# Performance work log

Measured on AMD Instinct MI355X. Metric: run time of the kernel, lower is better.

## Reference

```python
import jax, jax.numpy as jnp
import numpy as np
import itertools

GRID = 256          # voxel grid extent per axis (coords in [0, GRID))
KSIZE = 3           # kernel_size
OFFSETS = np.array(list(itertools.product(range(KSIZE), repeat=3)), dtype=np.int32) - (KSIZE // 2)  # [27,3]


def setup_inputs() -> dict:
    key = jax.random.key(0)
    k1, k2, k3 = jax.random.split(key, 3)
    N, Cin, Cout = 262144, 64, 64
    coords = jax.random.randint(k1, (N, 3), 0, GRID, dtype=jnp.int32)
    feats = jax.random.normal(k2, (N, Cin), dtype=jnp.float32)
    kernel = jax.random.normal(k3, (KSIZE ** 3, Cin, Cout), dtype=jnp.float32) * 0.02
    return {"coords": coords, "feats": feats, "kernel": kernel}


def reference(coords, feats, kernel):
    # Submanifold sparse conv3d: out[i] = sum_k feats[j_k(i)] @ kernel[k]
    # where coords[j_k(i)] == coords[i] + offset_k (if such a point exists).
    N = coords.shape[0]
    Cout = kernel.shape[-1]
    # Hash table: linearized voxel -> point index (-1 if empty).
    lin = (coords[:, 0] * GRID + coords[:, 1]) * GRID + coords[:, 2]
    table = jnp.full((GRID ** 3,), -1, dtype=jnp.int32).at[lin].set(
        jnp.arange(N, dtype=jnp.int32))
    out = jnp.zeros((N, Cout), dtype=feats.dtype)
    for k in range(KSIZE ** 3):
        off = jnp.asarray(OFFSETS[k])              # [3]
        nc = coords + off[None, :]                 # neighbor coords [N,3]
        in_bounds = jnp.all((nc >= 0) & (nc < GRID), axis=1)
        nlin = (nc[:, 0] * GRID + nc[:, 1]) * GRID + nc[:, 2]
        idx = table[jnp.clip(nlin, 0, GRID ** 3 - 1)]
        valid = in_bounds & (idx >= 0)
        g = feats[jnp.where(valid, idx, 0)] * valid[:, None].astype(feats.dtype)  # [N,Cin]
        out = out + g @ kernel[k]                  # [N,Cout]
    return out
```

## Files before the change

### kernel.cpp

```cpp
#include <hip/hip_runtime.h>

#define VGRID 256
#define N_TAPS 27
#define CIN 64
#define COUT 64
#define PAIR_CAP 32768
#define CNT_STRIDE 16
#define LCAP 64

typedef __attribute__((ext_vector_type(8))) short short8;
typedef __attribute__((ext_vector_type(4))) float float4v;

__device__ __forceinline__ short f2bf(float x) {
    unsigned u = __builtin_bit_cast(unsigned, x);
    unsigned r = (u + 0x7FFF + ((u >> 16) & 1)) >> 16;
    return (short)r;
}

__global__ void build_table_kernel(const int* __restrict__ coords,
                                   int* __restrict__ table, int n) {
    int i = blockIdx.x * blockDim.x + threadIdx.x;
    if (i >= n) return;
    int cx = coords[i * 3 + 0];
    int cy = coords[i * 3 + 1];
    int cz = coords[i * 3 + 2];
    int lin = (cx * VGRID + cy) * VGRID + cz;
    atomicMax(&table[lin], i);
}

__global__ void __launch_bounds__(256) probe_kernel(
        const int* __restrict__ coords, const int* __restrict__ table,
        int* __restrict__ counters, int2* __restrict__ pairs,
        int* __restrict__ jc, int n) {
    __shared__ int lcnt[26];
    __shared__ int lbase[26];
    __shared__ int2 lpairs[26][LCAP];

    int t = threadIdx.x;
    int i = blockIdx.x * 256 + t;
    if (t < 26) lcnt[t] = 0;
    __syncthreads();

    if (i < n) {
        int cx = coords[i * 3 + 0];
        int cy = coords[i * 3 + 1];
        int cz = coords[i * 3 + 2];
        int idxs[N_TAPS];
#pragma unroll
        for (int k = 0; k < N_TAPS; ++k) {
            int ox = k / 9 - 1, oy = (k / 3) % 3 - 1, oz = k % 3 - 1;
            int nx = cx + ox, ny = cy + oy, nz = cz + oz;
            bool v = ((unsigned)nx < VGRID) && ((unsigned)ny < VGRID) &&
                     ((unsigned)nz < VGRID);
            idxs[k] = v ? table[(nx * VGRID + ny) * VGRID + nz] : -1;
        }
        jc[i] = idxs[13];
#pragma unroll
        for (int k = 0; k < N_TAPS; ++k) {
            if (k == 13) continue;
            if (idxs[k] >= 0) {
                int kidx = k - (k > 13);
                int pos = atomicAdd(&lcnt[kidx], 1);
                if (pos < LCAP) lpairs[kidx][pos] = make_int2(i, idxs[k]);
            }
        }
    }
    __syncthreads();

    if (t < 26) {
        int c = lcnt[t];
        if (c > LCAP) c = LCAP;
        lcnt[t] = c;
        lbase[t] = atomicAdd(&counters[t * CNT_STRIDE], c);
    }
    __syncthreads();

    int wave = t >> 6, lane = t & 63;
    for (int k = wave; k < 26; k += 4) {
        int c = lcnt[k];
        if (lane < c) {
            int pos = lbase[k] + lane;
            if (pos < PAIR_CAP) pairs[(size_t)k * PAIR_CAP + pos] = lpairs[k][lane];
        }
    }
}

__global__ void __launch_bounds__(256) center_gemm_kernel(
        const float* __restrict__ feats, const float* __restrict__ weights,
        const int* __restrict__ jc, float* __restrict__ out, int n) {
    __shared__ short a_lds[64][CIN + 8];
    int base = blockIdx.x * 64;
    int t = threadIdx.x;

    {
        int r = t >> 2;
        int seg = (t & 3) * 16;
        int row = base + r;
        int j = (row < n) ? jc[row] : 0;
        const float4* src = (const float4*)(feats + (size_t)j * CIN + seg);
#pragma unroll
        for (int q = 0; q < 4; ++q) {
            float4 v = src[q];
            a_lds[r][seg + q * 4 + 0] = f2bf(v.x);
            a_lds[r][seg + q * 4 + 1] = f2bf(v.y);
            a_lds[r][seg + q * 4 + 2] = f2bf(v.z);
            a_lds[r][seg + q * 4 + 3] = f2bf(v.w);
        }
    }
    __syncthreads();

    int wave = t >> 6, lane = t & 63;
    int quad = lane >> 4, m = lane & 15;
    const float* W = weights + 13 * CIN * COUT;
    int row0 = wave * 16;

#pragma unroll
    for (int nt = 0; nt < 4; ++nt) {
        float4v acc = {0.f, 0.f, 0.f, 0.f};
        int nn = nt * 16 + m;
#pragma unroll
        for (int ks = 0; ks < 2; ++ks) {
            short8 a = *(const short8*)&a_lds[row0 + m][ks * 32 + quad * 8];
            short8 b;
#pragma unroll
            for (int j2 = 0; j2 < 8; ++j2) {
                int ci = ks * 32 + quad * 8 + j2;
                b[j2] = f2bf(W[ci * COUT + nn]);
            }
            acc = __builtin_amdgcn_mfma_f32_16x16x32_bf16(a, b, acc, 0, 0, 0);
        }
#pragma unroll
        for (int r2 = 0; r2 < 4; ++r2) {
            int orow = base + row0 + quad * 4 + r2;
            if (orow < n) out[(size_t)orow * COUT + nn] = acc[r2];
        }
    }
}

__global__ void __launch_bounds__(256) scatter_gemm_kernel(
        const float* __restrict__ feats, const float* __restrict__ weights,
        const int* __restrict__ counters, const int2* __restrict__ pairs,
        float* __restrict__ out) {
    __shared__ short a_lds[16][CIN + 8];
    __shared__ int i_arr[16];

    int kidx = blockIdx.y;
    int tap = kidx + (kidx >= 13);
    int cnt = counters[kidx * CNT_STRIDE];
    if (cnt > PAIR_CAP) cnt = PAIR_CAP;
    int ntiles = (cnt + 15) >> 4;
    const float* W = weights + (size_t)tap * CIN * COUT;
    const int2* P = pairs + (size_t)kidx * PAIR_CAP;

    int t = threadIdx.x;
    int wave = t >> 6, lane = t & 63;
    int quad = lane >> 4, m = lane & 15;

    for (int tile = blockIdx.x; tile < ntiles; tile += gridDim.x) {
        int tbase = tile * 16;
        int rem = cnt - tbase;
        if (rem > 16) rem = 16;

        if (t < 16) i_arr[t] = (t < rem) ? P[tbase + t].x : -1;
        {
            int r = t >> 4, q = t & 15;
            int j = (r < rem) ? P[tbase + r].y : -1;
            float4 v = {0.f, 0.f, 0.f, 0.f};
            if (j >= 0) v = *(const float4*)(feats + (size_t)j * CIN + q * 4);
            a_lds[r][q * 4 + 0] = f2bf(v.x);
            a_lds[r][q * 4 + 1] = f2bf(v.y);
            a_lds[r][q * 4 + 2] = f2bf(v.z);
            a_lds[r][q * 4 + 3] = f2bf(v.w);
        }
        __syncthreads();

        float4v acc = {0.f, 0.f, 0.f, 0.f};
        int nn = wave * 16 + m;
#pragma unroll
        for (int ks = 0; ks < 2; ++ks) {
            short8 a = *(const short8*)&a_lds[m][ks * 32 + quad * 8];
            short8 b;
#pragma unroll
            for (int j2 = 0; j2 < 8; ++j2) {
                int ci = ks * 32 + quad * 8 + j2;
                b[j2] = f2bf(W[ci * COUT + nn]);
            }
            acc = __builtin_amdgcn_mfma_f32_16x16x32_bf16(a, b, acc, 0, 0, 0);
        }
#pragma unroll
        for (int r2 = 0; r2 < 4; ++r2) {
            int row = quad * 4 + r2;
            int i = i_arr[row];
            if (i >= 0) atomicAdd(&out[(size_t)i * COUT + nn], acc[r2]);
        }
        __syncthreads();
    }
}

extern "C" void kernel_launch(void* const* d_in, const int* in_sizes, int n_in,
                              void* d_out, int out_size, void* d_ws, size_t ws_size,
                              hipStream_t stream) {
    const int* coords = (const int*)d_in[0];
    const float* feats = (const float*)d_in[1];
    const float* weights = (const float*)d_in[2];
    float* out = (float*)d_out;

    int n = in_sizes[0] / 3;

    char* ws = (char*)d_ws;
    size_t table_bytes = (size_t)VGRID * VGRID * VGRID * sizeof(int);
    int* table = (int*)ws;
    int* counters = (int*)(ws + table_bytes);
    int* jc = (int*)(ws + table_bytes + 26 * CNT_STRIDE * 4);
    int2* pairs = (int2*)(ws + table_bytes + 26 * CNT_STRIDE * 4 + (size_t)n * 4);

    hipMemsetAsync(table, 0xFF, table_bytes, stream);
    hipMemsetAsync(counters, 0, 26 * CNT_STRIDE * sizeof(int), stream);

    int bt_blocks = (n + 255) / 256;
    build_table_kernel<<<bt_blocks, 256, 0, stream>>>(coords, table, n);

    int pr_blocks = (n + 255) / 256;
    probe_kernel<<<pr_blocks, 256, 0, stream>>>(coords, table, counters, pairs, jc, n);

    int cg_blocks = (n + 63) / 64;
    center_gemm_kernel<<<cg_blocks, 256, 0, stream>>>(feats, weights, jc, out, n);

    dim3 sg_grid(64, 26);
    scatter_gemm_kernel<<<sg_grid, 256, 0, stream>>>(feats, weights, counters, pairs, out);
}
```

Measured before the change: 237.6 us.

## Replace full table memset with occupancy bitmap, pre-convert weights, widen scatter tiles

The 64MB memset of the dense voxel table is replaced by a 2MB occupancy bitmap memset plus a kernel that resets only the table entries for occupied voxels. The probe checks the bitmap before reading the table. Weights are converted once to transposed bf16 so the GEMMs load short8 vectors directly instead of converting per element. The scatter GEMM processes 64-row tiles with 4 N-tiles per wave on a larger grid, and PAIR_CAP is halved, which risks dropping pairs if any tap exceeds 16384.

Result: slower. 250.5 us (+5.4%).

```diff
diff --git a/kernel.cpp b/kernel.cpp
--- a/kernel.cpp
+++ b/kernel.cpp
@@ -4,12 +4,12 @@
 #define N_TAPS 27
 #define CIN 64
 #define COUT 64
-#define PAIR_CAP 32768
+#define PAIR_CAP 16384
 #define CNT_STRIDE 16
 #define LCAP 64
 
-typedef __attribute__((ext_vector_type(8))) short short8;
-typedef __attribute__((ext_vector_type(4))) float float4v;
+typedef short short8 __attribute__((ext_vector_type(8)));
+typedef float float4v __attribute__((ext_vector_type(4)));
 
 __device__ __forceinline__ short f2bf(float x) {
     unsigned u = __builtin_bit_cast(unsigned, x);
@@ -17,19 +17,36 @@
     return (short)r;
 }
 
-__global__ void build_table_kernel(const int* __restrict__ coords,
-                                   int* __restrict__ table, int n) {
+__global__ void init_table_kernel(const int* __restrict__ coords,
+                                  int* __restrict__ table, int n) {
     int i = blockIdx.x * blockDim.x + threadIdx.x;
     if (i >= n) return;
-    int cx = coords[i * 3 + 0];
-    int cy = coords[i * 3 + 1];
-    int cz = coords[i * 3 + 2];
-    int lin = (cx * VGRID + cy) * VGRID + cz;
+    int lin = (coords[i * 3 + 0] * VGRID + coords[i * 3 + 1]) * VGRID + coords[i * 3 + 2];
+    table[lin] = -1;
+}
+
+__global__ void build_table_kernel(const int* __restrict__ coords,
+                                   int* __restrict__ table,
+                                   unsigned* __restrict__ bits, int n) {
+    int i = blockIdx.x * blockDim.x + threadIdx.x;
+    if (i >= n) return;
+    int lin = (coords[i * 3 + 0] * VGRID + coords[i * 3 + 1]) * VGRID + coords[i * 3 + 2];
     atomicMax(&table[lin], i);
+    atomicOr(&bits[lin >> 5], 1u << (lin & 31));
+}
+
+__global__ void wconvert_kernel(const float* __restrict__ W,
+                                short* __restrict__ Wt) {
+    int tap = blockIdx.x;
+    for (int e = threadIdx.x; e < CIN * COUT; e += 256) {
+        int ci = e >> 6, co = e & 63;
+        Wt[((size_t)tap * COUT + co) * CIN + ci] = f2bf(W[((size_t)tap * CIN + ci) * COUT + co]);
+    }
 }
 
 __global__ void __launch_bounds__(256) probe_kernel(
         const int* __restrict__ coords, const int* __restrict__ table,
+        const unsigned* __restrict__ bits,
         int* __restrict__ counters, int2* __restrict__ pairs,
         int* __restrict__ jc, int n) {
     __shared__ int lcnt[26];
@@ -50,9 +67,12 @@
         for (int k = 0; k < N_TAPS; ++k) {
             int ox = k / 9 - 1, oy = (k / 3) % 3 - 1, oz = k % 3 - 1;
             int nx = cx + ox, ny = cy + oy, nz = cz + oz;
+            int nlin = (nx * VGRID + ny) * VGRID + nz;
+            if (k == 13) { idxs[k] = table[nlin]; continue; }
             bool v = ((unsigned)nx < VGRID) && ((unsigned)ny < VGRID) &&
                      ((unsigned)nz < VGRID);
-            idxs[k] = v ? table[(nx * VGRID + ny) * VGRID + nz] : -1;
+            bool occ = v && ((bits[(unsigned)nlin >> 5] >> (nlin & 31)) & 1);
+            idxs[k] = occ ? table[nlin] : -1;
         }
         jc[i] = idxs[13];
 #pragma unroll
@@ -86,7 +106,7 @@
 }
 
 __global__ void __launch_bounds__(256) center_gemm_kernel(
-        const float* __restrict__ feats, const float* __restrict__ weights,
+        const float* __restrict__ feats, const short* __restrict__ Wt,
         const int* __restrict__ jc, float* __restrict__ out, int n) {
     __shared__ short a_lds[64][CIN + 8];
     int base = blockIdx.x * 64;
@@ -111,7 +131,7 @@
 
     int wave = t >> 6, lane = t & 63;
     int quad = lane >> 4, m = lane & 15;
-    const float* W = weights + 13 * CIN * COUT;
+    const short* W13 = Wt + 13 * CIN * COUT;
     int row0 = wave * 16;
 
 #pragma unroll
@@ -121,12 +141,7 @@
 #pragma unroll
         for (int ks = 0; ks < 2; ++ks) {
             short8 a = *(const short8*)&a_lds[row0 + m][ks * 32 + quad * 8];
-            short8 b;
-#pragma unroll
-            for (int j2 = 0; j2 < 8; ++j2) {
-                int ci = ks * 32 + quad * 8 + j2;
-                b[j2] = f2bf(W[ci * COUT + nn]);
-            }
+            short8 b = *(const short8*)(W13 + (size_t)nn * CIN + ks * 32 + quad * 8);
             acc = __builtin_amdgcn_mfma_f32_16x16x32_bf16(a, b, acc, 0, 0, 0);
         }
 #pragma unroll
@@ -138,18 +153,18 @@
 }
 
 __global__ void __launch_bounds__(256) scatter_gemm_kernel(
-        const float* __restrict__ feats, const float* __restrict__ weights,
+        const float* __restrict__ feats, const short* __restrict__ Wt,
         const int* __restrict__ counters, const int2* __restrict__ pairs,
         float* __restrict__ out) {
-    __shared__ short a_lds[16][CIN + 8];
-    __shared__ int i_arr[16];
+    __shared__ short a_lds[64][CIN + 8];
+    __shared__ int i_arr[64];
 
     int kidx = blockIdx.y;
     int tap = kidx + (kidx >= 13);
     int cnt = counters[kidx * CNT_STRIDE];
     if (cnt > PAIR_CAP) cnt = PAIR_CAP;
-    int ntiles = (cnt + 15) >> 4;
-    const float* W = weights + (size_t)tap * CIN * COUT;
+    int ntiles = (cnt + 63) >> 6;
+    const short* W = Wt + (size_t)tap * CIN * COUT;
     const int2* P = pairs + (size_t)kidx * PAIR_CAP;
 
     int t = threadIdx.x;
@@ -157,41 +172,43 @@
     int quad = lane >> 4, m = lane & 15;
 
     for (int tile = blockIdx.x; tile < ntiles; tile += gridDim.x) {
-        int tbase = tile * 16;
+        int tbase = tile * 64;
         int rem = cnt - tbase;
-        if (rem > 16) rem = 16;
-
-        if (t < 16) i_arr[t] = (t < rem) ? P[tbase + t].x : -1;
+        if (rem > 64) rem = 64;
+
+        if (t < 64) i_arr[t] = (t < rem) ? P[tbase + t].x : -1;
         {
-            int r = t >> 4, q = t & 15;
+            int r = t >> 2;
+            int seg = (t & 3) * 16;
             int j = (r < rem) ? P[tbase + r].y : -1;
-            float4 v = {0.f, 0.f, 0.f, 0.f};
-            if (j >= 0) v = *(const float4*)(feats + (size_t)j * CIN + q * 4);
-            a_lds[r][q * 4 + 0] = f2bf(v.x);
-            a_lds[r][q * 4 + 1] = f2bf(v.y);
-            a_lds[r][q * 4 + 2] = f2bf(v.z);
-            a_lds[r][q * 4 + 3] = f2bf(v.w);
+#pragma unroll
+            for (int q = 0; q < 4; ++q) {
+                float4 v = {0.f, 0.f, 0.f, 0.f};
+                if (j >= 0) v = *(const float4*)(feats + (size_t)j * CIN + seg + q * 4);
+                a_lds[r][seg + q * 4 + 0] = f2bf(v.x);
+                a_lds[r][seg + q * 4 + 1] = f2bf(v.y);
+                a_lds[r][seg + q * 4 + 2] = f2bf(v.z);
+                a_lds[r][seg + q * 4 + 3] = f2bf(v.w);
+            }
         }
         __syncthreads();
 
-        float4v acc = {0.f, 0.f, 0.f, 0.f};
-        int nn = wave * 16 + m;
-#pragma unroll
-        for (int ks = 0; ks < 2; ++ks) {
-            short8 a = *(const short8*)&a_lds[m][ks * 32 + quad * 8];
-            short8 b;
-#pragma unroll
-            for (int j2 = 0; j2 < 8; ++j2) {
-                int ci = ks * 32 + quad * 8 + j2;
-                b[j2] = f2bf(W[ci * COUT + nn]);
-            }
-            acc = __builtin_amdgcn_mfma_f32_16x16x32_bf16(a, b, acc, 0, 0, 0);
-        }
-#pragma unroll
-        for (int r2 = 0; r2 < 4; ++r2) {
-            int row = quad * 4 + r2;
-            int i = i_arr[row];
-            if (i >= 0) atomicAdd(&out[(size_t)i * COUT + nn], acc[r2]);
+        int row0 = wave * 16;
+#pragma unroll
+        for (int nt = 0; nt < 4; ++nt) {
+            float4v acc = {0.f, 0.f, 0.f, 0.f};
+            int nn = nt * 16 + m;
+#pragma unroll
+            for (int ks = 0; ks < 2; ++ks) {
+                short8 a = *(const short8*)&a_lds[row0 + m][ks * 32 + quad * 8];
+                short8 b = *(const short8*)(W + (size_t)nn * CIN + ks * 32 + quad * 8);
+                acc = __builtin_amdgcn_mfma_f32_16x16x32_bf16(a, b, acc, 0, 0, 0);
+            }
+#pragma unroll
+            for (int r2 = 0; r2 < 4; ++r2) {
+                int i = i_arr[row0 + quad * 4 + r2];
+                if (i >= 0) atomicAdd(&out[(size_t)i * COUT + nn], acc[r2]);
+            }
         }
         __syncthreads();
     }
@@ -208,24 +225,26 @@
     int n = in_sizes[0] / 3;
 
     char* ws = (char*)d_ws;
-    size_t table_bytes = (size_t)VGRID * VGRID * VGRID * sizeof(int);
-    int* table = (int*)ws;
-    int* counters = (int*)(ws + table_bytes);
-    int* jc = (int*)(ws + table_bytes + 26 * CNT_STRIDE * 4);
-    int2* pairs = (int2*)(ws + table_bytes + 26 * CNT_STRIDE * 4 + (size_t)n * 4);
-
-    hipMemsetAsync(table, 0xFF, table_bytes, stream);
-    hipMemsetAsync(counters, 0, 26 * CNT_STRIDE * sizeof(int), stream);
-
-    int bt_blocks = (n + 255) / 256;
-    build_table_kernel<<<bt_blocks, 256, 0, stream>>>(coords, table, n);
-
-    int pr_blocks = (n + 255) / 256;
-    probe_kernel<<<pr_blocks, 256, 0, stream>>>(coords, table, counters, pairs, jc, n);
+    size_t BITMAP_BYTES = (size_t)VGRID * VGRID * VGRID / 8;
+    unsigned* bits = (unsigned*)ws;
+    int* counters = (int*)(ws + BITMAP_BYTES);
+    short* wbft = (short*)(ws + BITMAP_BYTES + 4096);
+    int* jc = (int*)(ws + BITMAP_BYTES + 4096 + 221184);
+    int2* pairs = (int2*)(ws + BITMAP_BYTES + 4096 + 221184 + (size_t)n * 4);
+    int* table = (int*)(ws + BITMAP_BYTES + 4096 + 221184 + (size_t)n * 4
+                        + (size_t)26 * PAIR_CAP * 8);
+
+    hipMemsetAsync(ws, 0, BITMAP_BYTES + 4096, stream);
+
+    int blocks = (n + 255) / 256;
+    init_table_kernel<<<blocks, 256, 0, stream>>>(coords, table, n);
+    build_table_kernel<<<blocks, 256, 0, stream>>>(coords, table, bits, n);
+    wconvert_kernel<<<N_TAPS, 256, 0, stream>>>(weights, wbft);
+    probe_kernel<<<blocks, 256, 0, stream>>>(coords, table, bits, counters, pairs, jc, n);
 
     int cg_blocks = (n + 63) / 64;
-    center_gemm_kernel<<<cg_blocks, 256, 0, stream>>>(feats, weights, jc, out, n);
-
-    dim3 sg_grid(64, 26);
-    scatter_gemm_kernel<<<sg_grid, 256, 0, stream>>>(feats, weights, counters, pairs, out);
-}
+    center_gemm_kernel<<<cg_blocks, 256, 0, stream>>>(feats, wbft, jc, out, n);
+
+    dim3 sg_grid(96, 26);
+    scatter_gemm_kernel<<<sg_grid, 256, 0, stream>>>(feats, wbft, counters, pairs, out);
+}
```
